# Kernel tuning notes

Hardware: AMD Instinct MI355X
Metric: run time of the kernel (lower is better)

The kernel has to match this reference:

```python
import jax, jax.numpy as jnp
import numpy as np

NEG = -10000.0
B, S, E, H, V, T = 64, 512, 300, 512, 100000, 12
START, STOP = T - 2, T - 1


def setup_inputs() -> dict:
    key = jax.random.key(0)
    ks = jax.random.split(key, 14)
    sc = 1.0 / np.sqrt(H)
    tokens = jax.random.randint(ks[0], (B, S), 0, V, dtype=jnp.int32)
    lengths = jax.random.randint(ks[1], (B,), S // 2, S + 1, dtype=jnp.int32)
    W_emb = jax.random.normal(ks[2], (V, E), jnp.float32) * 0.1
    W_ih_f = jax.random.uniform(ks[3], (4 * H, E), jnp.float32, -sc, sc)
    W_hh_f = jax.random.uniform(ks[4], (4 * H, H), jnp.float32, -sc, sc)
    b_f = jax.random.uniform(ks[5], (4 * H,), jnp.float32, -sc, sc)
    W_ih_b = jax.random.uniform(ks[6], (4 * H, E), jnp.float32, -sc, sc)
    W_hh_b = jax.random.uniform(ks[7], (4 * H, H), jnp.float32, -sc, sc)
    b_b = jax.random.uniform(ks[8], (4 * H,), jnp.float32, -sc, sc)
    h0 = jax.random.normal(ks[9], (2, B, H), jnp.float32)
    c0 = jax.random.normal(ks[10], (2, B, H), jnp.float32)
    W_out = jax.random.uniform(ks[11], (T, 2 * H), jnp.float32, -sc, sc)
    b_out = jax.random.uniform(ks[12], (T,), jnp.float32, -sc, sc)
    trans = jax.random.normal(ks[13], (T, T), jnp.float32)
    trans = trans.at[START, :].set(NEG).at[:, STOP].set(NEG)
    return {"tokens": tokens, "lengths": lengths, "W_emb": W_emb,
            "W_ih_f": W_ih_f, "W_hh_f": W_hh_f, "b_f": b_f,
            "W_ih_b": W_ih_b, "W_hh_b": W_hh_b, "b_b": b_b,
            "h0": h0, "c0": c0, "W_out": W_out, "b_out": b_out,
            "transitions": trans}


def _lstm(xW, W_hh, h0, c0):
    # xW: [S, B, 4H] = x @ W_ih.T + b (precomputed GEMM outside the scan)
    def step(carry, xw):
        h, c = carry
        g = xw + h @ W_hh.T
        i, f, gg, o = jnp.split(g, 4, axis=-1)  # torch gate order i,f,g,o
        i, f, o = jax.nn.sigmoid(i), jax.nn.sigmoid(f), jax.nn.sigmoid(o)
        c = f * c + i * jnp.tanh(gg)
        h = o * jnp.tanh(c)
        return (h, c), h
    _, hs = jax.lax.scan(step, (h0, c0), xW)
    return hs  # [S, B, H]


def reference(tokens, lengths, W_emb, W_ih_f, W_hh_f, b_f,
              W_ih_b, W_hh_b, b_b, h0, c0, W_out, b_out, transitions):
    # --- BiLSTM encoder ---
    x = W_emb[tokens].transpose(1, 0, 2)          # [S, B, E]
    hf = _lstm(x @ W_ih_f.T + b_f, W_hh_f, h0[0], c0[0])
    hb = _lstm(x[::-1] @ W_ih_b.T + b_b, W_hh_b, h0[1], c0[1])[::-1]
    feats = jnp.concatenate([hf, hb], axis=-1) @ W_out.T + b_out  # [S, B, T]
    # --- CRF forward algorithm (log partition) ---
    alpha0 = jnp.full((B, T), NEG, feats.dtype).at[:, START].set(0.0)
    mask = jnp.arange(S)[:, None] < lengths[None, :]  # [S, B]

    def crf_step(alpha, inp):
        feat, m = inp  # [B,T], [B]
        # next_tag_var[b, next, prev] = alpha[b,prev] + trans[next,prev] + emit[b,next]
        nv = alpha[:, None, :] + transitions[None, :, :] + feat[:, :, None]
        new = jax.nn.logsumexp(nv, axis=2)
        return jnp.where(m[:, None], new, alpha), None

    alpha, _ = jax.lax.scan(crf_step, alpha0, (feats, mask))
    terminal = alpha + transitions[STOP]
    return jnp.mean(jax.nn.logsumexp(terminal, axis=1))
```

## Files before the change

### kernel.cpp

```cpp
#include <hip/hip_runtime.h>
#include <hip/hip_bf16.h>

constexpr int B_ = 64, S_ = 512, E_ = 300, H_ = 512, T_ = 12;
constexpr int G4 = 4 * H_;
constexpr int KPADX = 320;
constexpr int KTOT = KPADX + H_;
constexpr int KC_TOT = KTOT / 32;
constexpr int KC_X = KPADX / 32;
constexpr int NT16 = G4 / 16;
constexpr float NEGV = -10000.0f;
constexpr int ASTR = 840;
constexpr unsigned SENT = 0xFFFFFFFFu;

typedef __attribute__((ext_vector_type(8))) short bf16x8_t;
typedef __attribute__((ext_vector_type(4))) float f32x4_t;
typedef __attribute__((ext_vector_type(4))) unsigned u32x4_t;

constexpr size_t WC_OFF = 0;
constexpr size_t WC_BYTES = (size_t)2 * NT16 * KC_TOT * 64 * 8 * 2;
constexpr size_t XC_OFF = WC_OFF + WC_BYTES;
constexpr size_t XC_BYTES = (size_t)S_ * B_ * KPADX * 2;
constexpr size_t HH_OFF = XC_OFF + XC_BYTES;
constexpr size_t HH_BYTES = (size_t)2 * (S_ + 1) * B_ * H_ * 2;
constexpr size_t FE_OFF = HH_OFF + HH_BYTES;
constexpr size_t FE_BYTES = (size_t)S_ * B_ * T_ * 4;
constexpr size_t LSE_OFF = FE_OFF + FE_BYTES;
constexpr size_t CHK_OFF = FE_OFF;

#define BAR_LDS() do {                                         \
    asm volatile("s_waitcnt lgkmcnt(0)" ::: "memory");         \
    __builtin_amdgcn_s_barrier();                              \
    __builtin_amdgcn_sched_barrier(0);                         \
  } while (0)

__global__ void prep_kernel(const float* __restrict__ Wih_f, const float* __restrict__ Whh_f,
                            const float* __restrict__ Wih_b, const float* __restrict__ Whh_b,
                            const float* __restrict__ h0,
                            const int* __restrict__ tokens, const float* __restrict__ Wemb,
                            char* __restrict__ ws) {
  __hip_bfloat16* wc = (__hip_bfloat16*)(ws + WC_OFF);
  __hip_bfloat16* xc = (__hip_bfloat16*)(ws + XC_OFF);
  __hip_bfloat16* hh = (__hip_bfloat16*)(ws + HH_OFF);
  const int WCN = 2 * NT16 * KC_TOT * 64;
  const int H0N = 2 * B_ * H_;
  const int XCN = S_ * B_ * (KPADX / 8);
  const int SFD = (S_ * B_ * H_ * 2) / 16;
  int idx = blockIdx.x * 256 + threadIdx.x;
  if (idx < WCN) {
    int lane = idx & 63;
    int r = idx >> 6;
    int kc = r % KC_TOT; r /= KC_TOT;
    int tt = r % NT16;
    int dir = r / NT16;
    int n16 = lane & 15, quad = lane >> 4;
    int nt = tt >> 2, gate = tt & 3;
    int j = gate * H_ + nt * 16 + n16;
    int k0 = kc * 32 + quad * 8;
    const float* Wih = dir ? Wih_b : Wih_f;
    const float* Whh = dir ? Whh_b : Whh_f;
    __hip_bfloat16* dst = wc + (size_t)idx * 8;
    #pragma unroll
    for (int jj = 0; jj < 8; jj++) {
      int k = k0 + jj;
      float f;
      if (k < E_) f = Wih[(size_t)j * E_ + k];
      else if (k < KPADX) f = 0.f;
      else f = Whh[(size_t)j * H_ + (k - KPADX)];
      dst[jj] = __float2bfloat16(f);
    }
  } else if (idx < WCN + H0N) {
    int i = idx - WCN;
    int dir = i / (B_ * H_), rem = i % (B_ * H_);
    hh[(size_t)dir * (S_ + 1) * B_ * H_ + rem] = __float2bfloat16(h0[i]);
  } else if (idx < WCN + H0N + XCN) {
    int i = idx - WCN - H0N;
    int c8 = i % 40, sb = i / 40;
    int s = sb >> 6, b = sb & 63;
    int k0 = c8 * 8;
    const float* src = Wemb + (size_t)tokens[(size_t)b * S_ + s] * E_;
    __hip_bfloat16 v[8];
    if (k0 + 8 <= E_) {
      float4 f0 = *(const float4*)(src + k0);
      float4 f1 = *(const float4*)(src + k0 + 4);
      v[0] = __float2bfloat16(f0.x); v[1] = __float2bfloat16(f0.y);
      v[2] = __float2bfloat16(f0.z); v[3] = __float2bfloat16(f0.w);
      v[4] = __float2bfloat16(f1.x); v[5] = __float2bfloat16(f1.y);
      v[6] = __float2bfloat16(f1.z); v[7] = __float2bfloat16(f1.w);
    } else {
      #pragma unroll
      for (int jj = 0; jj < 8; jj++) {
        int k = k0 + jj;
        v[jj] = __float2bfloat16(k < E_ ? src[k] : 0.f);
      }
    }
    *(uint4*)(xc + (size_t)sb * KPADX + k0) = *(const uint4*)v;
  } else if (idx < WCN + H0N + XCN + 2 * SFD) {
    int i = idx - WCN - H0N - XCN;
    int dir = i / SFD, j = i % SFD;
    uint4* dst = (uint4*)(hh + (size_t)dir * (S_ + 1) * B_ * H_ + B_ * H_);
    uint4 sv; sv.x = SENT; sv.y = SENT; sv.z = SENT; sv.w = SENT;
    dst[j] = sv;
  } else if (idx < WCN + H0N + XCN + 2 * SFD + 256) {
    ((unsigned*)(ws + CHK_OFF))[idx - (WCN + H0N + XCN + 2 * SFD)] = SENT;
  }
}

__launch_bounds__(256, 1)
__global__ void lstm_persist(const float* __restrict__ bias_f,
                             const float* __restrict__ bias_b,
                             const float* __restrict__ c0,
                             char* __restrict__ ws) {
  __shared__ short pool[16 * ASTR];
  __shared__ float gl[4 * 16 * 17];
  const int bid = blockIdx.x;
  const int g = bid & 7, nt = bid >> 3, dir = g >> 2, mt = g & 3;
  const int tid = threadIdx.x, lane = tid & 63, wv = tid >> 6;
  const int quad = lane >> 4, l16 = lane & 15;
  const __hip_bfloat16* wc = (const __hip_bfloat16*)(ws + WC_OFF);
  const __hip_bfloat16* xc = (const __hip_bfloat16*)(ws + XC_OFF);
  const __hip_bfloat16* hhb = (const __hip_bfloat16*)(ws + HH_OFF);
  unsigned* hh_u = (unsigned*)(ws + HH_OFF);

  bf16x8_t bfr[KC_TOT];
  #pragma unroll
  for (int kc = 0; kc < KC_TOT; kc++) {
    size_t boff = (((size_t)dir * NT16 + (nt * 4 + wv)) * KC_TOT + kc) * 64 + lane;
    bfr[kc] = *(const bf16x8_t*)(wc + boff * 8);
  }
  const int bo = tid >> 4, hl = tid & 15;
  const int b = mt * 16 + bo, hg = nt * 16 + hl;
  float c = c0[(size_t)(dir * B_ + b) * H_ + hg];
  const float* bias = dir ? bias_b : bias_f;
  const float bi_i = bias[0 * H_ + hg], bi_f = bias[1 * H_ + hg];
  const float bi_g = bias[2 * H_ + hg], bi_o = bias[3 * H_ + hg];

  int fastu;
  {
    unsigned* chk = (unsigned*)(ws + CHK_OFF);
    unsigned* chkl = (unsigned*)pool;
    if (tid == 0) {
      unsigned xcc;
      asm volatile("s_getreg_b32 %0, hwreg(HW_REG_XCC_ID)" : "=s"(xcc));
      __hip_atomic_store(chk + bid, xcc & 0xFu, __ATOMIC_RELAXED,
                         __HIP_MEMORY_SCOPE_AGENT);
    }
    unsigned myv;
    for (;;) {
      myv = __hip_atomic_load(chk + tid, __ATOMIC_RELAXED, __HIP_MEMORY_SCOPE_AGENT);
      if (myv != SENT) break;
      __builtin_amdgcn_s_sleep(4);
    }
    chkl[tid] = myv;
    __syncthreads();
    bool f = true;
    unsigned mask = 0;
    for (int gg = 0; gg < 8; gg++) {
      unsigned v0 = chkl[gg];
      f = f && (v0 < 32u);
      mask |= (1u << (v0 & 31u));
      for (int m = 1; m < 32; m++) f = f && (chkl[gg + 8 * m] == v0);
    }
    f = f && (__popc(mask) == 8);
    fastu = __builtin_amdgcn_readfirstlane(f ? 1 : 0);
    __syncthreads();
  }

  {
    int spos0 = dir ? (S_ - 1) : 0;
    for (int i = tid; i < 16 * 40; i += 256) {
      int row = i / 40, c8 = i % 40;
      *(uint4*)(pool + row * ASTR + c8 * 8) =
          *(const uint4*)(xc + ((size_t)spos0 * B_ + mt * 16 + row) * KPADX + c8 * 8);
    }
  }
  __syncthreads();

  int wdog = 0;
  for (int s = 0; s < S_; s++) {
    f32x4_t acc = (f32x4_t)(0.f);
    #pragma unroll
    for (int kc = 0; kc < KC_X; kc++) {
      bf16x8_t af = *(const bf16x8_t*)(pool + l16 * ASTR + kc * 32 + quad * 8);
      acc = __builtin_amdgcn_mfma_f32_16x16x32_bf16(af, bfr[kc], acc, 0, 0, 0);
    }
    const u32x4_t* pbase = (const u32x4_t*)(hhb +
        ((size_t)(dir * (S_ + 1) + s) * B_ + mt * 16) * H_);
    u32x4_t t0, t1, t2, t3;
    bool got = false;
    if (fastu && !wdog) {
      const u32x4_t* q0 = pbase + tid;
      bool ok0 = false;
      for (int tries = 0; tries < 16384; ++tries) {
        asm volatile("global_load_dwordx4 %0, %1, off sc0\n\t"
                     "s_waitcnt vmcnt(0)"
                     : "=&v"(t0) : "v"(q0) : "memory");
        if (t0[0] != SENT && t0[1] != SENT && t0[2] != SENT && t0[3] != SENT) {
          ok0 = true; break;
        }
        __builtin_amdgcn_s_sleep(1);
      }
      if (ok0) {
        const u32x4_t* q1 = pbase + tid + 256;
        const u32x4_t* q2 = pbase + tid + 512;
        const u32x4_t* q3 = pbase + tid + 768;
        for (int tries = 0; tries < 16384; ++tries) {
          asm volatile("global_load_dwordx4 %0, %3, off sc0\n\t"
                       "global_load_dwordx4 %1, %4, off sc0\n\t"
                       "global_load_dwordx4 %2, %5, off sc0\n\t"
                       "s_waitcnt vmcnt(0)"
                       : "=&v"(t1), "=&v"(t2), "=&v"(t3)
                       : "v"(q1), "v"(q2), "v"(q3)
                       : "memory");
          bool ok = t1[0] != SENT && t1[1] != SENT && t1[2] != SENT && t1[3] != SENT &&
                    t2[0] != SENT && t2[1] != SENT && t2[2] != SENT && t2[3] != SENT &&
                    t3[0] != SENT && t3[1] != SENT && t3[2] != SENT && t3[3] != SENT;
          if (ok) { got = true; break; }
          __builtin_amdgcn_s_sleep(1);
        }
      }
      if (!got) wdog = 1;
    }
    if (!got) {
      const unsigned long long* qq = (const unsigned long long*)pbase;
      u32x4_t tt[4];
      bool ok = false;
      while (!ok) {
        ok = true;
        #pragma unroll
        for (int k = 0; k < 4; k++) {
          int i = tid + k * 256;
          unsigned long long a0 = __hip_atomic_load(qq + 2 * i, __ATOMIC_RELAXED,
                                                    __HIP_MEMORY_SCOPE_AGENT);
          unsigned long long a1 = __hip_atomic_load(qq + 2 * i + 1, __ATOMIC_RELAXED,
                                                    __HIP_MEMORY_SCOPE_AGENT);
          tt[k][0] = (unsigned)a0; tt[k][1] = (unsigned)(a0 >> 32);
          tt[k][2] = (unsigned)a1; tt[k][3] = (unsigned)(a1 >> 32);
          ok = ok && tt[k][0] != SENT && tt[k][1] != SENT &&
                     tt[k][2] != SENT && tt[k][3] != SENT;
        }
        if (!ok) __builtin_amdgcn_s_sleep(1);
      }
      t0 = tt[0]; t1 = tt[1]; t2 = tt[2]; t3 = tt[3];
    }
    u32x4_t xpf0, xpf1, xpf2;
    const bool xok = (s + 1 < S_);
    if (xok) {
      int sposn = dir ? (S_ - 2 - s) : (s + 1);
      const u32x4_t* xq = (const u32x4_t*)xc;
      int i0 = tid, i1 = tid + 256, i2 = tid + 512;
      xpf0 = xq[((size_t)sposn * B_ + mt * 16 + i0 / 40) * 40 + i0 % 40];
      xpf1 = xq[((size_t)sposn * B_ + mt * 16 + i1 / 40) * 40 + i1 % 40];
      if (i2 < 640)
        xpf2 = xq[((size_t)sposn * B_ + mt * 16 + i2 / 40) * 40 + i2 % 40];
    }
    {
      int r0 = tid >> 6, c0v = tid & 63;
      *(u32x4_t*)(pool + r0 * ASTR + KPADX + c0v * 8) = t0;
      int i1 = tid + 256; int r1 = i1 >> 6, c1v = i1 & 63;
      *(u32x4_t*)(pool + r1 * ASTR + KPADX + c1v * 8) = t1;
      int i2 = tid + 512; int r2 = i2 >> 6, c2v = i2 & 63;
      *(u32x4_t*)(pool + r2 * ASTR + KPADX + c2v * 8) = t2;
      int i3 = tid + 768; int r3 = i3 >> 6, c3v = i3 & 63;
      *(u32x4_t*)(pool + r3 * ASTR + KPADX + c3v * 8) = t3;
    }
    BAR_LDS();
    #pragma unroll
    for (int kc = KC_X; kc < KC_TOT; kc++) {
      bf16x8_t af = *(const bf16x8_t*)(pool + l16 * ASTR + kc * 32 + quad * 8);
      acc = __builtin_amdgcn_mfma_f32_16x16x32_bf16(af, bfr[kc], acc, 0, 0, 0);
    }
    #pragma unroll
    for (int r = 0; r < 4; r++)
      gl[(wv * 16 + quad * 4 + r) * 17 + l16] = acc[r];
    BAR_LDS();
    float gi = gl[(0 * 16 + bo) * 17 + hl] + bi_i;
    float gf = gl[(1 * 16 + bo) * 17 + hl] + bi_f;
    float gg = gl[(2 * 16 + bo) * 17 + hl] + bi_g;
    float go = gl[(3 * 16 + bo) * 17 + hl] + bi_o;
    float ii = 1.f / (1.f + __expf(-gi));
    float ff = 1.f / (1.f + __expf(-gf));
    float gt = 1.f - 2.f / (1.f + __expf(2.f * gg));
    float oo = 1.f / (1.f + __expf(-go));
    c = ff * c + ii * gt;
    float hv2 = oo * (1.f - 2.f / (1.f + __expf(2.f * c)));
    float hn = __shfl_xor(hv2, 1, 64);
    if ((hl & 1) == 0) {
      unsigned short ulo = __builtin_bit_cast(unsigned short, __float2bfloat16(hv2));
      unsigned short uhi = __builtin_bit_cast(unsigned short, __float2bfloat16(hn));
      unsigned pk = ((unsigned)uhi << 16) | (unsigned)ulo;
      size_t uidx = (((size_t)(dir * (S_ + 1) + s + 1) * B_ + b) * H_ + hg) >> 1;
      if (fastu) {
        asm volatile("global_store_dword %0, %1, off sc0\n\t"
                     "s_waitcnt expcnt(0)"
                     :: "v"(hh_u + uidx), "v"(pk) : "memory");
      } else {
        __hip_atomic_store(hh_u + uidx, pk, __ATOMIC_RELAXED,
                           __HIP_MEMORY_SCOPE_AGENT);
      }
    }
    if (xok) {
      int i0 = tid, i1 = tid + 256, i2 = tid + 512;
      *(u32x4_t*)(pool + (i0 / 40) * ASTR + (i0 % 40) * 8) = xpf0;
      *(u32x4_t*)(pool + (i1 / 40) * ASTR + (i1 % 40) * 8) = xpf1;
      if (i2 < 640)
        *(u32x4_t*)(pool + (i2 / 40) * ASTR + (i2 % 40) * 8) = xpf2;
    }
    BAR_LDS();
  }
}

__launch_bounds__(256)
__global__ void feats_kernel(const float* __restrict__ Wout,
                             const float* __restrict__ bout,
                             char* __restrict__ ws) {
  __shared__ float wl[12 * 1032];
  const int s = blockIdx.x, tid = threadIdx.x;
  for (int i = tid; i < 12 * 1024 / 4; i += 256) {
    int idx4 = i * 4;
    int t = idx4 >> 10, k = idx4 & 1023;
    *(float4*)(wl + t * 1032 + k) = *(const float4*)(Wout + idx4);
  }
  __syncthreads();
  const __hip_bfloat16* hh = (const __hip_bfloat16*)(ws + HH_OFF);
  float* fe = (float*)(ws + FE_OFF);
  int b = tid >> 2, tg = tid & 3, t0 = tg * 3;
  const __hip_bfloat16* hf = hh + (size_t)(0 * (S_ + 1) + s + 1) * B_ * H_ + (size_t)b * H_;
  const __hip_bfloat16* hb = hh + (size_t)(1 * (S_ + 1) + (S_ - s)) * B_ * H_ + (size_t)b * H_;
  float a0 = 0.f, a1 = 0.f, a2 = 0.f;
  for (int half = 0; half < 2; half++) {
    const __hip_bfloat16* hp = half ? hb : hf;
    int wof = half * 512;
    for (int k = 0; k < 512; k += 8) {
      uint4 raw = *(const uint4*)(hp + k);
      const __hip_bfloat16* hv = (const __hip_bfloat16*)&raw;
      float hfl[8];
      #pragma unroll
      for (int j = 0; j < 8; j++) hfl[j] = __bfloat162float(hv[j]);
      #pragma unroll
      for (int j = 0; j < 8; j++) {
        a0 += hfl[j] * wl[(t0 + 0) * 1032 + wof + k + j];
        a1 += hfl[j] * wl[(t0 + 1) * 1032 + wof + k + j];
        a2 += hfl[j] * wl[(t0 + 2) * 1032 + wof + k + j];
      }
    }
  }
  float* o = fe + ((size_t)b * S_ + s) * T_;
  o[t0 + 0] = a0 + bout[t0 + 0];
  o[t0 + 1] = a1 + bout[t0 + 1];
  o[t0 + 2] = a2 + bout[t0 + 2];
}

__launch_bounds__(64)
__global__ void crf_kernel(const int* __restrict__ lengths,
                           const float* __restrict__ trans,
                           char* __restrict__ ws) {
  const int b = blockIdx.x, lane = threadIdx.x;
  const float* fe = (const float*)(ws + FE_OFF);
  float* lse = (float*)(ws + LSE_OFF);
  const float* fb = fe + (size_t)b * S_ * T_;
  float tr[12];
  #pragma unroll
  for (int p = 0; p < 12; p++) tr[p] = (lane < 12) ? trans[lane * 12 + p] : 0.f;
  float tstop = (lane < 12) ? trans[11 * 12 + lane] : 0.f;
  float alpha = (lane == 10) ? 0.f : NEGV;
  const int len = lengths[b];
  float feat = (lane < 12) ? fb[lane] : 0.f;
  for (int s = 0; s < S_; s++) {
    float fn = (lane < 12 && s + 1 < S_) ? fb[(size_t)(s + 1) * T_ + lane] : 0.f;
    float av[12];
    #pragma unroll
    for (int p = 0; p < 12; p++) av[p] = __shfl(alpha, p, 64) + tr[p];
    float mx = av[0];
    #pragma unroll
    for (int p = 1; p < 12; p++) mx = fmaxf(mx, av[p]);
    float sum = 0.f;
    #pragma unroll
    for (int p = 0; p < 12; p++) sum += __expf(av[p] - mx);
    float nw = mx + __logf(sum) + feat;
    if (s < len && lane < 12) alpha = nw;
    feat = fn;
  }
  float tv = (lane < 12) ? (alpha + tstop) : -3.0e38f;
  float mx = tv;
  #pragma unroll
  for (int off = 32; off > 0; off >>= 1) mx = fmaxf(mx, __shfl_xor(mx, off, 64));
  float sum = __expf(tv - mx);
  #pragma unroll
  for (int off = 32; off > 0; off >>= 1) sum += __shfl_xor(sum, off, 64);
  if (lane == 0) lse[b] = mx + __logf(sum);
}

__global__ void final_kernel(char* __restrict__ ws, float* __restrict__ out) {
  const float* lse = (const float*)(ws + LSE_OFF);
  float v = lse[threadIdx.x];
  #pragma unroll
  for (int off = 32; off > 0; off >>= 1) v += __shfl_xor(v, off, 64);
  if (threadIdx.x == 0) out[0] = v * (1.f / 64.f);
}

extern "C" void kernel_launch(void* const* d_in, const int* in_sizes, int n_in,
                              void* d_out, int out_size, void* d_ws, size_t ws_size,
                              hipStream_t stream) {
  (void)in_sizes; (void)n_in; (void)out_size; (void)ws_size;
  const int* tokens = (const int*)d_in[0];
  const int* lengths = (const int*)d_in[1];
  const float* Wemb = (const float*)d_in[2];
  const float* Wih_f = (const float*)d_in[3];
  const float* Whh_f = (const float*)d_in[4];
  const float* b_f = (const float*)d_in[5];
  const float* Wih_b = (const float*)d_in[6];
  const float* Whh_b = (const float*)d_in[7];
  const float* b_b = (const float*)d_in[8];
  const float* h0 = (const float*)d_in[9];
  const float* c0 = (const float*)d_in[10];
  const float* Wout = (const float*)d_in[11];
  const float* bout = (const float*)d_in[12];
  const float* trans = (const float*)d_in[13];
  char* ws = (char*)d_ws;
  float* out = (float*)d_out;

  int prep_items = 2 * NT16 * KC_TOT * 64 + 2 * B_ * H_ + S_ * B_ * (KPADX / 8)
                 + 2 * (S_ * B_ * H_ * 2) / 16 + 256;
  hipLaunchKernelGGL(prep_kernel, dim3((prep_items + 255) / 256), dim3(256), 0, stream,
                     Wih_f, Whh_f, Wih_b, Whh_b, h0, tokens, Wemb, ws);
  hipLaunchKernelGGL(lstm_persist, dim3(256), dim3(256), 0, stream, b_f, b_b, c0, ws);
  hipLaunchKernelGGL(feats_kernel, dim3(S_), dim3(256), 0, stream, Wout, bout, ws);
  hipLaunchKernelGGL(crf_kernel, dim3(B_), dim3(64), 0, stream, lengths, trans, ws);
  hipLaunchKernelGGL(final_kernel, dim3(1), dim3(64), 0, stream, ws, out);
}
```

Baseline: 1.453 ms.

## Interleave gate columns per wave so LSTM cell update avoids block barrier

Weight packing is reordered so each wave's 16 MFMA output columns hold all four gates for four hidden units, letting each wave finish the cell update from its own LDS slice with only a waitcnt instead of a block-wide barrier. The spin-wait on the previous hidden state now issues all four loads together each try instead of polling one chunk before fetching the rest. This removes one __syncthreads per timestep from the serial recurrence and shortens the poll latency, at the cost of more memory traffic per retry while waiting.

```diff
diff --git a/kernel.cpp b/kernel.cpp
--- a/kernel.cpp
+++ b/kernel.cpp
@@ -11,6 +11,7 @@
 constexpr float NEGV = -10000.0f;
 constexpr int ASTR = 840;
 constexpr unsigned SENT = 0xFFFFFFFFu;
+constexpr int GLW = 16 * 17;
 
 typedef __attribute__((ext_vector_type(8))) short bf16x8_t;
 typedef __attribute__((ext_vector_type(4))) float f32x4_t;
@@ -53,8 +54,8 @@
     int tt = r % NT16;
     int dir = r / NT16;
     int n16 = lane & 15, quad = lane >> 4;
-    int nt = tt >> 2, gate = tt & 3;
-    int j = gate * H_ + nt * 16 + n16;
+    int nt = tt >> 2, wvq = tt & 3;
+    int j = (n16 >> 2) * H_ + nt * 16 + wvq * 4 + (n16 & 3);
     int k0 = kc * 32 + quad * 8;
     const float* Wih = dir ? Wih_b : Wih_f;
     const float* Whh = dir ? Whh_b : Whh_f;
@@ -111,7 +112,7 @@
                              const float* __restrict__ c0,
                              char* __restrict__ ws) {
   __shared__ short pool[16 * ASTR];
-  __shared__ float gl[4 * 16 * 17];
+  __shared__ float gl[4 * GLW];
   const int bid = blockIdx.x;
   const int g = bid & 7, nt = bid >> 3, dir = g >> 2, mt = g & 3;
   const int tid = threadIdx.x, lane = tid & 63, wv = tid >> 6;
@@ -127,8 +128,8 @@
     size_t boff = (((size_t)dir * NT16 + (nt * 4 + wv)) * KC_TOT + kc) * 64 + lane;
     bfr[kc] = *(const bf16x8_t*)(wc + boff * 8);
   }
-  const int bo = tid >> 4, hl = tid & 15;
-  const int b = mt * 16 + bo, hg = nt * 16 + hl;
+  const int batt = quad * 4 + (l16 >> 2), hcl = l16 & 3;
+  const int b = mt * 16 + batt, hg = nt * 16 + wv * 4 + hcl;
   float c = c0[(size_t)(dir * B_ + b) * H_ + hg];
   const float* bias = dir ? bias_b : bias_f;
   const float bi_i = bias[0 * H_ + hg], bi_f = bias[1 * H_ + hg];
@@ -189,34 +190,25 @@
     bool got = false;
     if (fastu && !wdog) {
       const u32x4_t* q0 = pbase + tid;
-      bool ok0 = false;
+      const u32x4_t* q1 = pbase + tid + 256;
+      const u32x4_t* q2 = pbase + tid + 512;
+      const u32x4_t* q3 = pbase + tid + 768;
       for (int tries = 0; tries < 16384; ++tries) {
-        asm volatile("global_load_dwordx4 %0, %1, off sc0\n\t"
-                     "s_waitcnt vmcnt(0)"
-                     : "=&v"(t0) : "v"(q0) : "memory");
-        if (t0[0] != SENT && t0[1] != SENT && t0[2] != SENT && t0[3] != SENT) {
-          ok0 = true; break;
-        }
+        asm volatile(
+            "global_load_dwordx4 %0, %4, off sc0\n\t"
+            "global_load_dwordx4 %1, %5, off sc0\n\t"
+            "global_load_dwordx4 %2, %6, off sc0\n\t"
+            "global_load_dwordx4 %3, %7, off sc0\n\t"
+            "s_waitcnt vmcnt(0)"
+            : "=&v"(t0), "=&v"(t1), "=&v"(t2), "=&v"(t3)
+            : "v"(q0), "v"(q1), "v"(q2), "v"(q3)
+            : "memory");
+        bool ok = t0[0] != SENT && t0[1] != SENT && t0[2] != SENT && t0[3] != SENT &&
+                  t1[0] != SENT && t1[1] != SENT && t1[2] != SENT && t1[3] != SENT &&
+                  t2[0] != SENT && t2[1] != SENT && t2[2] != SENT && t2[3] != SENT &&
+                  t3[0] != SENT && t3[1] != SENT && t3[2] != SENT && t3[3] != SENT;
+        if (ok) { got = true; break; }
         __builtin_amdgcn_s_sleep(1);
-      }
-      if (ok0) {
-        const u32x4_t* q1 = pbase + tid + 256;
-        const u32x4_t* q2 = pbase + tid + 512;
-        const u32x4_t* q3 = pbase + tid + 768;
-        for (int tries = 0; tries < 16384; ++tries) {
-          asm volatile("global_load_dwordx4 %0, %3, off sc0\n\t"
-                       "global_load_dwordx4 %1, %4, off sc0\n\t"
-                       "global_load_dwordx4 %2, %5, off sc0\n\t"
-                       "s_waitcnt vmcnt(0)"
-                       : "=&v"(t1), "=&v"(t2), "=&v"(t3)
-                       : "v"(q1), "v"(q2), "v"(q3)
-                       : "memory");
-          bool ok = t1[0] != SENT && t1[1] != SENT && t1[2] != SENT && t1[3] != SENT &&
-                    t2[0] != SENT && t2[1] != SENT && t2[2] != SENT && t2[3] != SENT &&
-                    t3[0] != SENT && t3[1] != SENT && t3[2] != SENT && t3[3] != SENT;
-          if (ok) { got = true; break; }
-          __builtin_amdgcn_s_sleep(1);
-        }
       }
       if (!got) wdog = 1;
     }
@@ -269,33 +261,37 @@
       bf16x8_t af = *(const bf16x8_t*)(pool + l16 * ASTR + kc * 32 + quad * 8);
       acc = __builtin_amdgcn_mfma_f32_16x16x32_bf16(af, bfr[kc], acc, 0, 0, 0);
     }
-    #pragma unroll
-    for (int r = 0; r < 4; r++)
-      gl[(wv * 16 + quad * 4 + r) * 17 + l16] = acc[r];
-    BAR_LDS();
-    float gi = gl[(0 * 16 + bo) * 17 + hl] + bi_i;
-    float gf = gl[(1 * 16 + bo) * 17 + hl] + bi_f;
-    float gg = gl[(2 * 16 + bo) * 17 + hl] + bi_g;
-    float go = gl[(3 * 16 + bo) * 17 + hl] + bi_o;
-    float ii = 1.f / (1.f + __expf(-gi));
-    float ff = 1.f / (1.f + __expf(-gf));
-    float gt = 1.f - 2.f / (1.f + __expf(2.f * gg));
-    float oo = 1.f / (1.f + __expf(-go));
-    c = ff * c + ii * gt;
-    float hv2 = oo * (1.f - 2.f / (1.f + __expf(2.f * c)));
-    float hn = __shfl_xor(hv2, 1, 64);
-    if ((hl & 1) == 0) {
-      unsigned short ulo = __builtin_bit_cast(unsigned short, __float2bfloat16(hv2));
-      unsigned short uhi = __builtin_bit_cast(unsigned short, __float2bfloat16(hn));
-      unsigned pk = ((unsigned)uhi << 16) | (unsigned)ulo;
-      size_t uidx = (((size_t)(dir * (S_ + 1) + s + 1) * B_ + b) * H_ + hg) >> 1;
-      if (fastu) {
-        asm volatile("global_store_dword %0, %1, off sc0\n\t"
-                     "s_waitcnt expcnt(0)"
-                     :: "v"(hh_u + uidx), "v"(pk) : "memory");
-      } else {
-        __hip_atomic_store(hh_u + uidx, pk, __ATOMIC_RELAXED,
-                           __HIP_MEMORY_SCOPE_AGENT);
+    {
+      float* glw = gl + wv * GLW;
+      #pragma unroll
+      for (int r = 0; r < 4; r++)
+        glw[l16 * 17 + quad * 4 + r] = acc[r];
+      asm volatile("s_waitcnt lgkmcnt(0)" ::: "memory");
+      __builtin_amdgcn_sched_barrier(0);
+      float gi = glw[(0 * 4 + hcl) * 17 + batt] + bi_i;
+      float gf = glw[(1 * 4 + hcl) * 17 + batt] + bi_f;
+      float gg = glw[(2 * 4 + hcl) * 17 + batt] + bi_g;
+      float go = glw[(3 * 4 + hcl) * 17 + batt] + bi_o;
+      float ii = 1.f / (1.f + __expf(-gi));
+      float ff = 1.f / (1.f + __expf(-gf));
+      float gt = 1.f - 2.f / (1.f + __expf(2.f * gg));
+      float oo = 1.f / (1.f + __expf(-go));
+      c = ff * c + ii * gt;
+      float hv2 = oo * (1.f - 2.f / (1.f + __expf(2.f * c)));
+      float hn = __shfl_xor(hv2, 1, 64);
+      if ((hcl & 1) == 0) {
+        unsigned short ulo = __builtin_bit_cast(unsigned short, __float2bfloat16(hv2));
+        unsigned short uhi = __builtin_bit_cast(unsigned short, __float2bfloat16(hn));
+        unsigned pk = ((unsigned)uhi << 16) | (unsigned)ulo;
+        size_t uidx = (((size_t)(dir * (S_ + 1) + s + 1) * B_ + b) * H_ + hg) >> 1;
+        if (fastu) {
+          asm volatile("global_store_dword %0, %1, off sc0\n\t"
+                       "s_waitcnt expcnt(0)"
+                       :: "v"(hh_u + uidx), "v"(pk) : "memory");
+        } else {
+          __hip_atomic_store(hh_u + uidx, pk, __ATOMIC_RELAXED,
+                             __HIP_MEMORY_SCOPE_AGENT);
+        }
       }
     }
     if (xok) {
```

New measurement: 1.325 ms. -8.8%, faster.
